# Optimization experiments

Hardware: AMD Instinct MI355X
Metric: run time of the kernel (lower is better)

Reference implementation:

```python
import jax, jax.numpy as jnp
import numpy as np

NA, NT, A_DIM, E_DIM, L_LABELS, STEPS = 1024, 1024, 128, 128, 128, 2


def setup_inputs() -> dict:
    key = jax.random.key(0)
    k1, k2, k3, k4, k5 = jax.random.split(key, 5)
    return {
        "inputs": jax.random.randint(k1, (NA, NT), 0, L_LABELS, dtype=jnp.int32),
        "first_a": jax.random.normal(k2, (NA, A_DIM), dtype=jnp.float32),
        "first_t": jax.random.normal(k3, (NT, E_DIM), dtype=jnp.float32),
        "Awij": jax.random.normal(k4, (L_LABELS, A_DIM, E_DIM), dtype=jnp.float32),
        "Awij2": jax.random.normal(k5, (L_LABELS, E_DIM, A_DIM), dtype=jnp.float32),
    }


def _mp_step(update_a, update_t, inputs, Awij, Awij2):
    L = Awij.shape[0]
    # Phase A: a[j] += sum_t update_t[t] @ Awij2[inputs[j, t]]
    # Pre-contract task states with every label's weight matrix, then use
    # per-label 0/1 adjacency masks as dense GEMMs (compute-bound form of the
    # per-edge gather-multiply-accumulate in the original while loops).
    t_proj = jnp.einsum('te,lea->tla', update_t, Awij2)  # [Nt, L, A]

    def body_a(acc, l):
        mask = (inputs == l).astype(update_a.dtype)      # [Na, Nt]
        return acc + mask @ t_proj[:, l, :], None

    msg_a, _ = jax.lax.scan(body_a, jnp.zeros_like(update_a), jnp.arange(L))
    new_a = update_a + msg_a

    # Phase T: t[k] += sum_j new_a[j] @ Awij[inputs[j, k]] (uses updated a,
    # matching the loop order in the original body)
    a_proj = jnp.einsum('ja,lae->jle', new_a, Awij)      # [Na, L, E]

    def body_t(acc, l):
        mask = (inputs == l).astype(update_t.dtype)      # [Na, Nt]
        return acc + mask.T @ a_proj[:, l, :], None

    msg_t, _ = jax.lax.scan(body_t, jnp.zeros_like(update_t), jnp.arange(L))
    return new_a, update_t + msg_t


def reference(inputs, first_a, first_t, Awij, Awij2):
    a, t = first_a, first_t
    for _ in range(STEPS):
        a, t = _mp_step(a, t, inputs, Awij, Awij2)
    na, a_dim = a.shape
    nt, e_dim = t.shape
    top = jnp.concatenate([a, jnp.zeros((na, e_dim), a.dtype)], axis=1)
    bot = jnp.concatenate([t, jnp.zeros((nt, a_dim), t.dtype)], axis=1)
    return jnp.concatenate([top, bot], axis=0)  # [Na+Nt, A+E]
```

## Files before the change

### kernel.cpp

```cpp
#include <hip/hip_runtime.h>
#include <hip/hip_bf16.h>
#include <stdint.h>


typedef short bf16x8 __attribute__((ext_vector_type(8)));
typedef float f32x4  __attribute__((ext_vector_type(4)));

#define GLD16(g, l) __builtin_amdgcn_global_load_lds( \
    (const __attribute__((address_space(1))) void*)(uintptr_t)(g), \
    (__attribute__((address_space(3))) void*)(uintptr_t)(l), 16, 0, 0)

#define BF_LO(v) __uint_as_float((v) << 16)
#define BF_HI(v) __uint_as_float((v) & 0xffff0000u)

static __device__ __forceinline__ uint32_t pk2(float lo, float hi) {
    __hip_bfloat16 h0 = __float2bfloat16(lo), h1 = __float2bfloat16(hi);
    return ((uint32_t)(*(uint16_t*)&h1) << 16) | (uint32_t)(*(uint16_t*)&h0);
}

__global__ __launch_bounds__(256) void transpose_int_kernel(const int* __restrict__ in,
                                                            int* __restrict__ out) {
    __shared__ int tile[32][33];
    int b = blockIdx.x;
    int tr = b >> 5, tc = b & 31;
    int r0 = tr * 32, c0 = tc * 32;
    int tx = threadIdx.x & 31, ty = threadIdx.x >> 5;
#pragma unroll
    for (int p = 0; p < 4; ++p)
        tile[ty + p * 8][tx] = in[(size_t)(r0 + ty + p * 8) * 1024 + c0 + tx];
    __syncthreads();
#pragma unroll
    for (int p = 0; p < 4; ++p) {
        int cc = ty + p * 8;
        out[(size_t)(c0 + cc) * 1024 + r0 + tx] = tile[tx][cc];
    }
}

__global__ __launch_bounds__(256) void transpose_w_kernel(const float* __restrict__ W2,
                                                          const float* __restrict__ W1,
                                                          uint16_t* __restrict__ O2T,
                                                          uint16_t* __restrict__ O1T) {
    __shared__ float tile[32][33];
    int b = blockIdx.x;
    const float* W = W2;
    uint16_t* O = O2T;
    if (b >= 2048) { b -= 2048; W = W1; O = O1T; }
    int l = b >> 4, sub = b & 15;
    int x0 = (sub >> 2) * 32, y0 = (sub & 3) * 32;
    int tx = threadIdx.x & 31, ty = threadIdx.x >> 5;
#pragma unroll
    for (int p = 0; p < 4; ++p)
        tile[ty + p * 8][tx] = W[(size_t)l * 16384 + (size_t)(x0 + ty + p * 8) * 128 + y0 + tx];
    __syncthreads();
#pragma unroll
    for (int p = 0; p < 4; ++p) {
        int yy = ty + p * 8;
        __hip_bfloat16 h = __float2bfloat16(tile[tx][yy]);
        O[(size_t)(l * 128 + y0 + yy) * 128 + x0 + tx] = *(uint16_t*)&h;
    }
}

__global__ __launch_bounds__(256) void init_out_kernel(const float* __restrict__ fa,
                                                       const float* __restrict__ ft,
                                                       float* __restrict__ out,
                                                       uint16_t* __restrict__ srcAb,
                                                       uint16_t* __restrict__ srcTb) {
    int i = blockIdx.x * 256 + threadIdx.x;
    int r = i >> 8, c = i & 255;
    float v = 0.f;
    if (c < 128) {
        v = (r < 1024) ? fa[(size_t)r * 128 + c] : ft[(size_t)(r - 1024) * 128 + c];
        __hip_bfloat16 h = __float2bfloat16(v);
        if (r < 1024) srcAb[(size_t)r * 128 + c] = *(uint16_t*)&h;
        else          srcTb[(size_t)(r - 1024) * 128 + c] = *(uint16_t*)&h;
    }
    out[i] = v;
}

__global__ __launch_bounds__(512, 2) void proj_kernel(const uint16_t* __restrict__ src,
                                                      const uint16_t* __restrict__ WT,
                                                      uint16_t* __restrict__ proj) {
    __shared__ uint16_t At[128 * 128];
    __shared__ uint16_t Bt[128 * 128];

    const int tid = threadIdx.x;
    const int lane = tid & 63, wv = tid >> 6;
    const int bid = blockIdx.x;
    const int virt = (bid & 7) * 128 + (bid >> 3);
    const int mt = virt & 7;
    const int nt = virt >> 3;
    const int wr = wv >> 2, wc = wv & 3;

    const int rr = lane >> 4;
    const int sx16 = lane & 15;
#pragma unroll
    for (int g = 0; g < 4; ++g) {
        int row = wv * 16 + g * 4 + rr;
        int sx = sx16 ^ (row & 15);
        GLD16((const char*)src + ((size_t)(mt * 128 + row) * 128 + sx * 8) * 2,
              (char*)At + (wv * 16 + g * 4) * 256);
        GLD16((const char*)WT + ((size_t)(nt * 128 + row) * 128 + sx * 8) * 2,
              (char*)Bt + (wv * 16 + g * 4) * 256);
    }
    __syncthreads();

    f32x4 acc[4][2] = {};
    const int q = lane >> 4, rl = lane & 15;
#pragma unroll
    for (int kk = 0; kk < 4; ++kk) {
        bf16x8 af[4], bfr[2];
#pragma unroll
        for (int m = 0; m < 4; ++m) {
            int row = wr * 64 + m * 16 + rl;
            int sw = (kk * 4 + q) ^ (row & 15);
            af[m] = *(const bf16x8*)((const char*)At + row * 256 + sw * 16);
        }
#pragma unroll
        for (int n = 0; n < 2; ++n) {
            int row = wc * 32 + n * 16 + rl;
            int sw = (kk * 4 + q) ^ (row & 15);
            bfr[n] = *(const bf16x8*)((const char*)Bt + row * 256 + sw * 16);
        }
#pragma unroll
        for (int m = 0; m < 4; ++m)
#pragma unroll
            for (int n = 0; n < 2; ++n)
                acc[m][n] = __builtin_amdgcn_mfma_f32_16x16x32_bf16(bfr[n], af[m], acc[m][n], 0, 0, 0);
    }

#pragma unroll
    for (int m = 0; m < 4; ++m)
#pragma unroll
        for (int n = 0; n < 2; ++n) {
            int mrow = mt * 128 + wr * 64 + m * 16 + rl;
            int ncol = nt * 128 + wc * 32 + n * 16 + q * 4;
            uint2 pk;
            pk.x = pk2(acc[m][n][0], acc[m][n][1]);
            pk.y = pk2(acc[m][n][2], acc[m][n][3]);
            *(uint2*)(proj + (size_t)mrow * 16384 + ncol) = pk;
        }
}

__global__ __launch_bounds__(512, 8) void gather_kernel(const int* __restrict__ labels,
                                                        const uint32_t* __restrict__ proj,
                                                        float* __restrict__ state,
                                                        uint16_t* __restrict__ mirror) {
    __shared__ uint16_t lab16[1024];
    __shared__ float red[8][128];
    const int j = blockIdx.x;
    const int tid = threadIdx.x;
    const int lane = tid & 63, wv = tid >> 6;

    lab16[tid] = (uint16_t)labels[(size_t)j * 1024 + tid];
    lab16[512 + tid] = (uint16_t)labels[(size_t)j * 1024 + 512 + tid];
    __syncthreads();

    float a0 = 0.f, a1 = 0.f, b0 = 0.f, b1 = 0.f;
    const uint32_t lane_u = (uint32_t)lane;
#pragma unroll 1
    for (int i = 0; i < 128; i += 8) {
        int t = wv * 128 + i;
        ushort4 L0 = *(const ushort4*)&lab16[t];
        ushort4 L1 = *(const ushort4*)&lab16[t + 4];
        const uint32_t* base = proj + (size_t)t * 8192 + lane_u;
        uint32_t v0 = base[(uint32_t)L0.x * 64];
        uint32_t v1 = base[8192u + (uint32_t)L0.y * 64];
        uint32_t v2 = base[16384u + (uint32_t)L0.z * 64];
        uint32_t v3 = base[24576u + (uint32_t)L0.w * 64];
        uint32_t v4 = base[32768u + (uint32_t)L1.x * 64];
        uint32_t v5 = base[40960u + (uint32_t)L1.y * 64];
        uint32_t v6 = base[49152u + (uint32_t)L1.z * 64];
        uint32_t v7 = base[57344u + (uint32_t)L1.w * 64];
        a0 += BF_LO(v0) + BF_LO(v1) + BF_LO(v2) + BF_LO(v3);
        a1 += BF_HI(v0) + BF_HI(v1) + BF_HI(v2) + BF_HI(v3);
        b0 += BF_LO(v4) + BF_LO(v5) + BF_LO(v6) + BF_LO(v7);
        b1 += BF_HI(v4) + BF_HI(v5) + BF_HI(v6) + BF_HI(v7);
    }
    float2 pr;
    pr.x = a0 + b0;
    pr.y = a1 + b1;
    *(float2*)&red[wv][lane * 2] = pr;
    __syncthreads();

    if (tid < 128) {
        float s = ((red[0][tid] + red[1][tid]) + (red[2][tid] + red[3][tid]))
                + ((red[4][tid] + red[5][tid]) + (red[6][tid] + red[7][tid]));
        float v = state[(size_t)j * 256 + tid] + s;
        state[(size_t)j * 256 + tid] = v;
        __hip_bfloat16 h = __float2bfloat16(v);
        mirror[(size_t)j * 128 + tid] = *(uint16_t*)&h;
    }
}

extern "C" void kernel_launch(void* const* d_in, const int* in_sizes, int n_in,
                              void* d_out, int out_size, void* d_ws, size_t ws_size,
                              hipStream_t stream) {
    const int*   inputs  = (const int*)d_in[0];
    const float* first_a = (const float*)d_in[1];
    const float* first_t = (const float*)d_in[2];
    const float* Awij    = (const float*)d_in[3];
    const float* Awij2   = (const float*)d_in[4];
    float* out = (float*)d_out;

    char* w = (char*)d_ws;
    int*      inputsT = (int*)(w);
    uint16_t* W2T     = (uint16_t*)(w + (4u << 20));
    uint16_t* W1T     = (uint16_t*)(w + (8u << 20));
    uint16_t* srcAb   = (uint16_t*)(w + (12u << 20));
    uint16_t* srcTb   = (uint16_t*)(w + (12u << 20) + (1u << 18));
    uint16_t* proj16  = (uint16_t*)(w + (16u << 20));
    if (ws_size < (48u << 20)) return;

    float* stateA = out;
    float* stateT = out + 1024 * 256;

    transpose_int_kernel<<<1024, 256, 0, stream>>>(inputs, inputsT);
    transpose_w_kernel<<<4096, 256, 0, stream>>>(Awij2, Awij, W2T, W1T);
    init_out_kernel<<<2048, 256, 0, stream>>>(first_a, first_t, out, srcAb, srcTb);

    for (int s = 0; s < 2; ++s) {
        proj_kernel<<<1024, 512, 0, stream>>>(srcTb, W2T, proj16);
        gather_kernel<<<1024, 512, 0, stream>>>(inputs, (const uint32_t*)proj16, stateA, srcAb);
        proj_kernel<<<1024, 512, 0, stream>>>(srcAb, W1T, proj16);
        gather_kernel<<<1024, 512, 0, stream>>>(inputsT, (const uint32_t*)proj16, stateT, srcTb);
    }
}
```

Measured before the change: 197.1 us.

## Split gather over task chunks with partial sums and separate reduce kernel

The gather kernel now splits each row's 1024 task positions into 8 chunks handled by separate 256-thread blocks. Each block writes partial sums to a workspace buffer, and a new reduce kernel adds them into the state and the bf16 mirror. This raises the block count from 1024 to 8192 to give more parallelism and latency hiding for the random-gather loads. In exchange it adds an extra launch per phase and a round trip of the partials through global memory.

Measured after the change: 170.1 us. 13.7% less time.

```diff
diff --git a/kernel.cpp b/kernel.cpp
--- a/kernel.cpp
+++ b/kernel.cpp
@@ -141,28 +141,29 @@
         }
 }
 
-__global__ __launch_bounds__(512, 8) void gather_kernel(const int* __restrict__ labels,
-                                                        const uint32_t* __restrict__ proj,
-                                                        float* __restrict__ state,
-                                                        uint16_t* __restrict__ mirror) {
-    __shared__ uint16_t lab16[1024];
-    __shared__ float red[8][128];
-    const int j = blockIdx.x;
+__global__ __launch_bounds__(256, 8) void gather_partial_kernel(
+    const int* __restrict__ labels,
+    const uint32_t* __restrict__ proj,
+    float* __restrict__ partial)
+{
+    __shared__ uint16_t lab16[128];
+    __shared__ float red[4][128];
+    const int bid = blockIdx.x;
+    const int j = bid >> 3, ts = bid & 7;
     const int tid = threadIdx.x;
     const int lane = tid & 63, wv = tid >> 6;
 
-    lab16[tid] = (uint16_t)labels[(size_t)j * 1024 + tid];
-    lab16[512 + tid] = (uint16_t)labels[(size_t)j * 1024 + 512 + tid];
+    if (tid < 128) lab16[tid] = (uint16_t)labels[(size_t)j * 1024 + ts * 128 + tid];
     __syncthreads();
 
     float a0 = 0.f, a1 = 0.f, b0 = 0.f, b1 = 0.f;
     const uint32_t lane_u = (uint32_t)lane;
+    const int t0 = ts * 128 + wv * 32;
 #pragma unroll 1
-    for (int i = 0; i < 128; i += 8) {
-        int t = wv * 128 + i;
-        ushort4 L0 = *(const ushort4*)&lab16[t];
-        ushort4 L1 = *(const ushort4*)&lab16[t + 4];
-        const uint32_t* base = proj + (size_t)t * 8192 + lane_u;
+    for (int i = 0; i < 32; i += 8) {
+        ushort4 L0 = *(const ushort4*)&lab16[wv * 32 + i];
+        ushort4 L1 = *(const ushort4*)&lab16[wv * 32 + i + 4];
+        const uint32_t* base = proj + (size_t)(t0 + i) * 8192 + lane_u;
         uint32_t v0 = base[(uint32_t)L0.x * 64];
         uint32_t v1 = base[8192u + (uint32_t)L0.y * 64];
         uint32_t v2 = base[16384u + (uint32_t)L0.z * 64];
@@ -183,13 +184,22 @@
     __syncthreads();
 
     if (tid < 128) {
-        float s = ((red[0][tid] + red[1][tid]) + (red[2][tid] + red[3][tid]))
-                + ((red[4][tid] + red[5][tid]) + (red[6][tid] + red[7][tid]));
-        float v = state[(size_t)j * 256 + tid] + s;
-        state[(size_t)j * 256 + tid] = v;
-        __hip_bfloat16 h = __float2bfloat16(v);
-        mirror[(size_t)j * 128 + tid] = *(uint16_t*)&h;
-    }
+        float s = (red[0][tid] + red[1][tid]) + (red[2][tid] + red[3][tid]);
+        partial[((size_t)j * 8 + ts) * 128 + tid] = s;
+    }
+}
+
+__global__ __launch_bounds__(256) void reduce_state_kernel(const float* __restrict__ partial,
+                                                           float* __restrict__ state,
+                                                           uint16_t* __restrict__ mirror) {
+    int i = blockIdx.x * 256 + threadIdx.x;
+    int j = i >> 7, c = i & 127;
+    const float* p = partial + (size_t)j * 1024 + c;
+    float s = ((p[0] + p[128]) + (p[256] + p[384])) + ((p[512] + p[640]) + (p[768] + p[896]));
+    float v = state[(size_t)j * 256 + c] + s;
+    state[(size_t)j * 256 + c] = v;
+    __hip_bfloat16 h = __float2bfloat16(v);
+    mirror[(size_t)j * 128 + c] = *(uint16_t*)&h;
 }
 
 extern "C" void kernel_launch(void* const* d_in, const int* in_sizes, int n_in,
@@ -207,9 +217,10 @@
     uint16_t* W2T     = (uint16_t*)(w + (4u << 20));
     uint16_t* W1T     = (uint16_t*)(w + (8u << 20));
     uint16_t* srcAb   = (uint16_t*)(w + (12u << 20));
-    uint16_t* srcTb   = (uint16_t*)(w + (12u << 20) + (1u << 18));
-    uint16_t* proj16  = (uint16_t*)(w + (16u << 20));
-    if (ws_size < (48u << 20)) return;
+    uint16_t* srcTb   = (uint16_t*)(w + (12u << 20) + (1u << 19));
+    float*    partial = (float*)(w + (13u << 20));
+    uint16_t* proj16  = (uint16_t*)(w + (20u << 20));
+    if (ws_size < (52u << 20)) return;
 
     float* stateA = out;
     float* stateT = out + 1024 * 256;
@@ -220,8 +231,10 @@
 
     for (int s = 0; s < 2; ++s) {
         proj_kernel<<<1024, 512, 0, stream>>>(srcTb, W2T, proj16);
-        gather_kernel<<<1024, 512, 0, stream>>>(inputs, (const uint32_t*)proj16, stateA, srcAb);
+        gather_partial_kernel<<<8192, 256, 0, stream>>>(inputs, (const uint32_t*)proj16, partial);
+        reduce_state_kernel<<<512, 256, 0, stream>>>(partial, stateA, srcAb);
         proj_kernel<<<1024, 512, 0, stream>>>(srcAb, W1T, proj16);
-        gather_kernel<<<1024, 512, 0, stream>>>(inputsT, (const uint32_t*)proj16, stateT, srcTb);
-    }
-}
+        gather_partial_kernel<<<8192, 256, 0, stream>>>(inputsT, (const uint32_t*)proj16, partial);
+        reduce_state_kernel<<<512, 256, 0, stream>>>(partial, stateT, srcTb);
+    }
+}
```
